# Performance work log

Hardware: AMD Instinct MI355X
Metric: run time of the kernel (lower is better)

## Reference

```python
import jax, jax.numpy as jnp
import numpy as np
import math

B, N, DIM = 4, 2048, 768
HEADS, DIM_HEAD = 12, 64
SCALE = math.sqrt(DIM_HEAD)


def setup_inputs() -> dict:
    key = jax.random.key(0)
    ks = jax.random.split(key, 5)
    inner = HEADS * DIM_HEAD
    x = jax.random.normal(ks[0], (B, N, DIM), dtype=jnp.float32)
    # Linear weights stored as [in, out] so y = x @ W (equivalent to torch Linear with W.T)
    w_q = jax.random.normal(ks[1], (DIM, inner), dtype=jnp.float32) * 0.02
    w_k = jax.random.normal(ks[2], (DIM, inner), dtype=jnp.float32) * 0.02
    w_v = jax.random.normal(ks[3], (DIM, inner), dtype=jnp.float32) * 0.02
    w_o = jax.random.normal(ks[4], (inner, DIM), dtype=jnp.float32) * 0.02
    b_o = jnp.zeros((DIM,), dtype=jnp.float32)
    return {"x": x, "w_q": w_q, "w_k": w_k, "w_v": w_v, "w_o": w_o, "b_o": b_o}


def _split_heads(t):
    # [b, n, h*d] -> [b, h, n, d]
    b, n, _ = t.shape
    return t.reshape(b, n, HEADS, DIM_HEAD).transpose(0, 2, 1, 3)


def reference(x, w_q, w_k, w_v, w_o, b_o):
    # context = x (self-attention, kv_include_self=False)
    q = _split_heads(x @ w_q)  # [b,h,n,d]
    k = _split_heads(x @ w_k)
    v = _split_heads(x @ w_v)
    scores = jnp.einsum("bhnd,bhmd->bhnm", q, k) / SCALE  # [b,h,n,n]
    attn = jax.nn.softmax(scores, axis=-1)  # dropout p=0 -> identity
    h = jnp.einsum("bhnm,bhmd->bhnd", attn, v)  # [b,h,n,d]
    H = h.transpose(0, 2, 1, 3).reshape(x.shape[0], x.shape[1], HEADS * DIM_HEAD)
    out = H @ w_o + b_o
    return out
```

## Files before the change

### kernel.cpp

```cpp
#include <hip/hip_runtime.h>
#include <hip/hip_bf16.h>
#include <cstdint>
#include <cstddef>

#define HEADS 12
#define DHEAD 64
#define SEQ   2048
#define DIMM  768
#define BATCH 4
#define MROWS (BATCH*SEQ)
#define BH    (BATCH*HEADS)
#define SCL_Q 0.18033688011112042f

typedef __attribute__((ext_vector_type(8))) short short8;
typedef __attribute__((ext_vector_type(4))) short short4v;
typedef __attribute__((ext_vector_type(4))) float floatx4;

__device__ __forceinline__ unsigned short f2bf(float f) {
    union { float f; uint32_t u; } v; v.f = f;
    uint32_t u = v.u;
    u += 0x7fffu + ((u >> 16) & 1u);
    return (unsigned short)(u >> 16);
}
__device__ __forceinline__ float bf2f(unsigned short h) {
    union { uint32_t u; float f; } v; v.u = ((uint32_t)h) << 16;
    return v.f;
}
__device__ __forceinline__ uint32_t pkbf(float a, float b) {
    __hip_bfloat162 h = __float22bfloat162_rn(make_float2(a, b));
    uint32_t u; __builtin_memcpy(&u, &h, 4); return u;
}
__device__ __forceinline__ float fexp2(float x) {
#if __has_builtin(__builtin_amdgcn_exp2f)
    return __builtin_amdgcn_exp2f(x);
#else
    return exp2f(x);
#endif
}

#if __has_builtin(__builtin_amdgcn_global_load_lds)
#define HAVE_GLDS 1
__device__ __forceinline__ void glds16(const unsigned short* g, unsigned short* l) {
    __builtin_amdgcn_global_load_lds(
        (const __attribute__((address_space(1))) unsigned int*)g,
        (__attribute__((address_space(3))) unsigned int*)l, 16, 0, 0);
}
#else
#define HAVE_GLDS 0
#endif

__device__ __forceinline__ int detect_f32(const uint32_t* xw, int tid) {
    __shared__ int cnt_;
    if (tid == 0) cnt_ = 0;
    __syncthreads();
    uint32_t w = xw[(size_t)(tid & 255) * 4096];
    float av = fabsf(bf2f((unsigned short)(w & 0xFFFFu)));
    atomicAdd(&cnt_, (av >= 9.0949e-13f && av <= 256.0f) ? 1 : 0);
    __syncthreads();
    return (cnt_ < 192) ? 1 : 0;
}

__global__ __launch_bounds__(256) void prep(
    const void* __restrict__ x,
    const void* __restrict__ wq, const void* __restrict__ wk,
    const void* __restrict__ wv, const void* __restrict__ wo,
    unsigned short* __restrict__ xc,
    unsigned short* __restrict__ wtq, unsigned short* __restrict__ wtk,
    unsigned short* __restrict__ wtv, unsigned short* __restrict__ wto)
{
    const int tid = threadIdx.x;
    const int isf32 = detect_f32((const uint32_t*)x, tid);
    const int blk = blockIdx.x;

    if (blk < 2304) {
        __shared__ unsigned short tile[32][33];
        const int m = blk / 576, rr = blk % 576;
        const void* src; unsigned short* dst;
        switch (m) {
            case 0: src = wq; dst = wtq; break;
            case 1: src = wk; dst = wtk; break;
            case 2: src = wv; dst = wtv; break;
            default: src = wo; dst = wto; break;
        }
        const float* srcf = (const float*)src;
        const unsigned short* srcs = (const unsigned short*)src;
        const int tx = tid & 31, ty = tid >> 5;
        const int k0 = (rr % 24) * 32;
        const int n0 = (rr / 24) * 32;
        #pragma unroll
        for (int it = 0; it < 4; it++) {
            int r = ty + it * 8;
            size_t idx = (size_t)(k0 + r) * DIMM + n0 + tx;
            tile[r][tx] = isf32 ? f2bf(srcf[idx]) : srcs[idx];
        }
        __syncthreads();
        #pragma unroll
        for (int it = 0; it < 4; it++) {
            int r = ty + it * 8;
            dst[(size_t)(n0 + r) * DIMM + k0 + tx] = tile[tx][r];
        }
    } else {
        const size_t i0 = ((size_t)(blk - 2304) * 256 + tid) * 8;
        if (isf32) {
            const float* xf = (const float*)x;
            float4 a = *(const float4*)&xf[i0];
            float4 b = *(const float4*)&xf[i0 + 4];
            short8 s = { (short)f2bf(a.x), (short)f2bf(a.y), (short)f2bf(a.z), (short)f2bf(a.w),
                         (short)f2bf(b.x), (short)f2bf(b.y), (short)f2bf(b.z), (short)f2bf(b.w) };
            *(short8*)&xc[i0] = s;
        } else {
            *(short8*)&xc[i0] = *(const short8*)&((const unsigned short*)x)[i0];
        }
    }
}

__global__ __launch_bounds__(256) void gemm_bt(
    const unsigned short* __restrict__ A,
    const unsigned short* __restrict__ Wt0,
    const unsigned short* __restrict__ Wt1,
    const unsigned short* __restrict__ Wt2,
    void* __restrict__ O0, void* __restrict__ O1, void* __restrict__ O2,
    const void* __restrict__ bias,
    const uint32_t* __restrict__ xsample,
    int mode_base)
{
    const int blk   = blockIdx.x;
    const int bmix  = blk & 63;
    const int inner = blk >> 6;
    int bnix, mode;
    if (mode_base == 0) { bnix = inner % 6; mode = inner / 6; }
    else                { bnix = inner;     mode = 3;         }

    const unsigned short* Wt = (mode == 1) ? Wt1 : (mode == 2) ? Wt2 : Wt0;
    void* OutV               = (mode == 1) ? O1  : (mode == 2) ? O2  : O0;
    unsigned short* Out16 = (unsigned short*)OutV;
    float* Outf           = (float*)OutV;

    int isf32 = 0;
    if (mode == 3) isf32 = detect_f32(xsample, threadIdx.x);

    __shared__ unsigned short As[128 * 64];
    __shared__ unsigned short Bs[128 * 64];

    const int tid  = threadIdx.x;
    const int wid  = tid >> 6;
    const int lane = tid & 63;
    const int l16  = lane & 15;
    const int quad = lane >> 4;
    const int wm   = wid & 1;
    const int wn   = wid >> 1;
    const int bm   = bmix * 128;
    const int bn   = bnix * 128;
    const bool swap = (mode != 2);

    floatx4 acc[4][4];
    #pragma unroll
    for (int i = 0; i < 4; i++)
        #pragma unroll
        for (int j = 0; j < 4; j++)
            acc[i][j] = floatx4{0.f, 0.f, 0.f, 0.f};

    for (int kk = 0; kk < DIMM; kk += 64) {
        #pragma unroll
        for (int t = 0; t < 4; t++) {
            const int c  = t * 256 + tid;
            const int r  = c >> 3;
            const int lc = (((c & 7) ^ (r & 7))) * 8;
#if HAVE_GLDS
            glds16(&A [(size_t)(bm + r) * DIMM + kk + lc], &As[(t * 256 + wid * 64) * 8]);
            glds16(&Wt[(size_t)(bn + r) * DIMM + kk + lc], &Bs[(t * 256 + wid * 64) * 8]);
#else
            *(short8*)&As[c * 8] = *(const short8*)&A [(size_t)(bm + r) * DIMM + kk + lc];
            *(short8*)&Bs[c * 8] = *(const short8*)&Wt[(size_t)(bn + r) * DIMM + kk + lc];
#endif
        }
        __syncthreads();
        #pragma unroll
        for (int ks = 0; ks < 2; ks++) {
            const int ph = ((ks * 4 + quad) ^ (l16 & 7)) * 8;
            short8 xa[4], wb[4];
            #pragma unroll
            for (int t = 0; t < 4; t++)
                xa[t] = *(const short8*)&As[(wm * 64 + t * 16 + l16) * 64 + ph];
            #pragma unroll
            for (int t = 0; t < 4; t++)
                wb[t] = *(const short8*)&Bs[(wn * 64 + t * 16 + l16) * 64 + ph];
            if (swap) {
                #pragma unroll
                for (int mt = 0; mt < 4; mt++)
                    #pragma unroll
                    for (int nt = 0; nt < 4; nt++)
                        acc[mt][nt] = __builtin_amdgcn_mfma_f32_16x16x32_bf16(
                            wb[mt], xa[nt], acc[mt][nt], 0, 0, 0);
            } else {
                #pragma unroll
                for (int mt = 0; mt < 4; mt++)
                    #pragma unroll
                    for (int nt = 0; nt < 4; nt++)
                        acc[mt][nt] = __builtin_amdgcn_mfma_f32_16x16x32_bf16(
                            xa[mt], wb[nt], acc[mt][nt], 0, 0, 0);
            }
        }
        __syncthreads();
    }

    if (!swap) {
        #pragma unroll
        for (int nt = 0; nt < 4; nt++) {
            const int gcol = bn + wn * 64 + nt * 16 + l16;
            #pragma unroll
            for (int mt = 0; mt < 4; mt++) {
                const int grow0 = bm + wm * 64 + mt * 16 + quad * 4;
                const int b = grow0 >> 11, n0 = grow0 & 2047;
                const int h = gcol >> 6,  d  = gcol & 63;
                size_t addr = ((size_t)(b * HEADS + h) * DHEAD + d) * SEQ + n0;
                short4v pk = { (short)f2bf(acc[mt][nt][0]), (short)f2bf(acc[mt][nt][1]),
                               (short)f2bf(acc[mt][nt][2]), (short)f2bf(acc[mt][nt][3]) };
                *(short4v*)&Out16[addr] = pk;
            }
        }
    } else {
        #pragma unroll
        for (int nt = 0; nt < 4; nt++) {
            const int grow = bm + wm * 64 + nt * 16 + l16;
            #pragma unroll
            for (int mt = 0; mt < 4; mt++) {
                const int gcol0 = bn + wn * 64 + mt * 16 + quad * 4;
                float v0 = acc[mt][nt][0], v1 = acc[mt][nt][1];
                float v2 = acc[mt][nt][2], v3 = acc[mt][nt][3];
                if (mode == 0) { v0 *= SCL_Q; v1 *= SCL_Q; v2 *= SCL_Q; v3 *= SCL_Q; }
                if (mode == 3) {
                    if (isf32) {
                        float4 bv = *(const float4*)&((const float*)bias)[gcol0];
                        float4 o = { v0 + bv.x, v1 + bv.y, v2 + bv.z, v3 + bv.w };
                        *(float4*)&Outf[(size_t)grow * DIMM + gcol0] = o;
                    } else {
                        const unsigned short* bb = &((const unsigned short*)bias)[gcol0];
                        short4v pk = { (short)f2bf(v0 + bf2f(bb[0])),
                                       (short)f2bf(v1 + bf2f(bb[1])),
                                       (short)f2bf(v2 + bf2f(bb[2])),
                                       (short)f2bf(v3 + bf2f(bb[3])) };
                        *(short4v*)&Out16[(size_t)grow * DIMM + gcol0] = pk;
                    }
                } else {
                    const int b = grow >> 11, n = grow & 2047;
                    const int h = gcol0 >> 6, d = gcol0 & 63;
                    size_t addr = ((size_t)(b * HEADS + h) * SEQ + n) * DHEAD + d;
                    short4v pk = { (short)f2bf(v0), (short)f2bf(v1),
                                   (short)f2bf(v2), (short)f2bf(v3) };
                    *(short4v*)&Out16[addr] = pk;
                }
            }
        }
    }
}

__global__ __launch_bounds__(256, 3) void attn(
    const unsigned short* __restrict__ Q,
    const unsigned short* __restrict__ K,
    const unsigned short* __restrict__ Vt,
    unsigned short* __restrict__ Hout)
{
    __shared__ unsigned short Ks[64 * 72];
    __shared__ unsigned short Vs[64 * 72];
    __shared__ unsigned short Ps[8][16 * 72];

    const int tid  = threadIdx.x;
    const int wid  = tid >> 6;
    const int lane = tid & 63;
    const int l16  = lane & 15;
    const int quad = lane >> 4;

    const int bh = blockIdx.x % BH;
    const int qt = blockIdx.x / BH;

    short8 qf[2][2];
    #pragma unroll
    for (int t = 0; t < 2; t++) {
        const int qrow = qt * 128 + wid * 32 + t * 16 + l16;
        const size_t qbase = ((size_t)bh * SEQ + qrow) * DHEAD;
        qf[t][0] = *(const short8*)&Q[qbase + quad * 8];
        qf[t][1] = *(const short8*)&Q[qbase + 32 + quad * 8];
    }

    const short8 ones = { (short)0x3F80, (short)0x3F80, (short)0x3F80, (short)0x3F80,
                          (short)0x3F80, (short)0x3F80, (short)0x3F80, (short)0x3F80 };

    floatx4 ot[2][4];
    floatx4 acc_l[2];
    #pragma unroll
    for (int t = 0; t < 2; t++) {
        acc_l[t] = floatx4{0.f, 0.f, 0.f, 0.f};
        #pragma unroll
        for (int i = 0; i < 4; i++) ot[t][i] = floatx4{0.f, 0.f, 0.f, 0.f};
    }

    const size_t kbase = (size_t)bh * SEQ * DHEAD;
    const size_t vbase = (size_t)bh * DHEAD * SEQ;

    short8 rk[2], rv[2];
    #pragma unroll
    for (int j = 0; j < 2; j++) {
        const int c = tid + j * 256, r = c >> 3, c8 = (c & 7) * 8;
        rk[j] = *(const short8*)&K[kbase + (size_t)r * DHEAD + c8];
        rv[j] = *(const short8*)&Vt[vbase + (size_t)r * SEQ + c8];
    }

    short8 vfr[2][4];
    short8 pfr[2][2];

    for (int kt = 0; kt < SEQ / 64; kt++) {
        if (kt > 0) {
            #pragma unroll
            for (int ks = 0; ks < 2; ks++) {
                #pragma unroll
                for (int dt = 0; dt < 4; dt++)
                    vfr[ks][dt] = *(const short8*)&Vs[(dt * 16 + l16) * 72 + ks * 32 + quad * 8];
                #pragma unroll
                for (int t = 0; t < 2; t++)
                    pfr[ks][t] = *(const short8*)&Ps[wid * 2 + t][l16 * 72 + ks * 32 + quad * 8];
            }
        }
        __syncthreads();
        #pragma unroll
        for (int j = 0; j < 2; j++) {
            const int c = tid + j * 256, r = c >> 3, c8 = (c & 7) * 8;
            *(short8*)&Ks[r * 72 + c8] = rk[j];
            *(short8*)&Vs[r * 72 + c8] = rv[j];
        }
        __syncthreads();
        if (kt + 1 < SEQ / 64) {
            #pragma unroll
            for (int j = 0; j < 2; j++) {
                const int c = tid + j * 256, r = c >> 3, c8 = (c & 7) * 8;
                rk[j] = *(const short8*)&K[kbase + (size_t)((kt + 1) * 64 + r) * DHEAD + c8];
                rv[j] = *(const short8*)&Vt[vbase + (size_t)r * SEQ + (kt + 1) * 64 + c8];
            }
        }

        uint2 pk[2][4];
        #pragma unroll
        for (int mt = 0; mt < 4; mt++) {
            short8 kf0 = *(const short8*)&Ks[(mt * 16 + l16) * 72 + quad * 8];
            short8 kf1 = *(const short8*)&Ks[(mt * 16 + l16) * 72 + 32 + quad * 8];
            #pragma unroll
            for (int t = 0; t < 2; t++) {
                floatx4 a = floatx4{0.f, 0.f, 0.f, 0.f};
                a = __builtin_amdgcn_mfma_f32_16x16x32_bf16(kf0, qf[t][0], a, 0, 0, 0);
                a = __builtin_amdgcn_mfma_f32_16x16x32_bf16(kf1, qf[t][1], a, 0, 0, 0);
                pk[t][mt] = (uint2){ pkbf(fexp2(a[0]), fexp2(a[1])),
                                     pkbf(fexp2(a[2]), fexp2(a[3])) };
            }
        }

        if (kt > 0) {
            #pragma unroll
            for (int ks = 0; ks < 2; ks++) {
                #pragma unroll
                for (int t = 0; t < 2; t++) {
                    #pragma unroll
                    for (int dt = 0; dt < 4; dt++)
                        ot[t][dt] = __builtin_amdgcn_mfma_f32_16x16x32_bf16(
                            vfr[ks][dt], pfr[ks][t], ot[t][dt], 0, 0, 0);
                    acc_l[t] = __builtin_amdgcn_mfma_f32_16x16x32_bf16(
                        ones, pfr[ks][t], acc_l[t], 0, 0, 0);
                }
            }
        }

        #pragma unroll
        for (int t = 0; t < 2; t++)
            #pragma unroll
            for (int mt = 0; mt < 4; mt++)
                *(uint2*)&Ps[wid * 2 + t][l16 * 72 + mt * 16 + quad * 4] = pk[t][mt];
    }

    {
        #pragma unroll
        for (int ks = 0; ks < 2; ks++) {
            #pragma unroll
            for (int dt = 0; dt < 4; dt++)
                vfr[ks][dt] = *(const short8*)&Vs[(dt * 16 + l16) * 72 + ks * 32 + quad * 8];
            #pragma unroll
            for (int t = 0; t < 2; t++)
                pfr[ks][t] = *(const short8*)&Ps[wid * 2 + t][l16 * 72 + ks * 32 + quad * 8];
        }
        #pragma unroll
        for (int ks = 0; ks < 2; ks++)
            #pragma unroll
            for (int t = 0; t < 2; t++) {
                #pragma unroll
                for (int dt = 0; dt < 4; dt++)
                    ot[t][dt] = __builtin_amdgcn_mfma_f32_16x16x32_bf16(
                        vfr[ks][dt], pfr[ks][t], ot[t][dt], 0, 0, 0);
                acc_l[t] = __builtin_amdgcn_mfma_f32_16x16x32_bf16(
                    ones, pfr[ks][t], acc_l[t], 0, 0, 0);
            }
    }

    const int b = bh / HEADS, h = bh % HEADS;
    #pragma unroll
    for (int t = 0; t < 2; t++) {
        const float inv_l = 1.0f / acc_l[t][0];
        unsigned short* Pw = Ps[wid * 2 + t];
        #pragma unroll
        for (int dt = 0; dt < 4; dt++) {
            uint2 pk2 = { pkbf(ot[t][dt][0] * inv_l, ot[t][dt][1] * inv_l),
                          pkbf(ot[t][dt][2] * inv_l, ot[t][dt][3] * inv_l) };
            *(uint2*)&Pw[l16 * 72 + dt * 16 + quad * 4] = pk2;
        }
        const int q_r   = lane >> 2;
        const int dpart = (lane & 3) * 16;
        short8 h0 = *(const short8*)&Pw[q_r * 72 + dpart];
        short8 h1 = *(const short8*)&Pw[q_r * 72 + dpart + 8];
        const int growg = b * SEQ + qt * 128 + wid * 32 + t * 16 + q_r;
        const size_t oaddr = (size_t)growg * DIMM + h * DHEAD + dpart;
        *(short8*)&Hout[oaddr] = h0;
        *(short8*)&Hout[oaddr + 8] = h1;
    }
}

extern "C" void kernel_launch(void* const* d_in, const int* in_sizes, int n_in,
                              void* d_out, int out_size, void* d_ws, size_t ws_size,
                              hipStream_t stream)
{
    (void)in_sizes; (void)n_in; (void)out_size;
    const void* x  = d_in[0];
    const void* wq = d_in[1];
    const void* wk = d_in[2];
    const void* wv = d_in[3];
    const void* wo = d_in[4];
    const void* bo = d_in[5];

    char* ws = (char*)d_ws;
    const size_t SZ_QKV = (size_t)MROWS * DIMM * sizeof(unsigned short);
    const size_t SZ_W   = (size_t)DIMM * DIMM * sizeof(unsigned short);
    const size_t need = 5 * SZ_QKV + 4 * SZ_W;
    if (ws_size < need) return;

    unsigned short* xc   = (unsigned short*)(ws);
    unsigned short* Qws  = (unsigned short*)(ws + 1 * SZ_QKV);
    unsigned short* Kws  = (unsigned short*)(ws + 2 * SZ_QKV);
    unsigned short* Vtws = (unsigned short*)(ws + 3 * SZ_QKV);
    unsigned short* Hws  = (unsigned short*)(ws + 4 * SZ_QKV);
    unsigned short* Wtq  = (unsigned short*)(ws + 5 * SZ_QKV);
    unsigned short* Wtk  = (unsigned short*)(ws + 5 * SZ_QKV + SZ_W);
    unsigned short* Wtv  = (unsigned short*)(ws + 5 * SZ_QKV + 2 * SZ_W);
    unsigned short* Wto  = (unsigned short*)(ws + 5 * SZ_QKV + 3 * SZ_W);

    hipLaunchKernelGGL(prep, dim3(2304 + MROWS * DIMM / 2048), dim3(256), 0, stream,
                       x, wq, wk, wv, wo, xc, Wtq, Wtk, Wtv, Wto);
    hipLaunchKernelGGL(gemm_bt, dim3(64 * 18), dim3(256), 0, stream,
                       xc, Wtq, Wtk, Wtv, (void*)Qws, (void*)Kws, (void*)Vtws,
                       bo, (const uint32_t*)x, 0);
    hipLaunchKernelGGL(attn, dim3(BH * (SEQ / 128)), dim3(256), 0, stream,
                       Qws, Kws, Vtws, Hws);
    hipLaunchKernelGGL(gemm_bt, dim3(64 * 6), dim3(256), 0, stream,
                       Hws, Wto, Wto, Wto, d_out, d_out, d_out,
                       bo, (const uint32_t*)x, 3);
}
```

Measured before the change: 244.9 us.

## Split GEMM into QKV and output kernels; use 256-row tiles for QKV

```diff
diff --git a/kernel.cpp b/kernel.cpp
--- a/kernel.cpp
+++ b/kernel.cpp
@@ -114,30 +114,158 @@
     }
 }
 
-__global__ __launch_bounds__(256) void gemm_bt(
+__global__ __launch_bounds__(256) void gemm_qkv(
     const unsigned short* __restrict__ A,
     const unsigned short* __restrict__ Wt0,
     const unsigned short* __restrict__ Wt1,
     const unsigned short* __restrict__ Wt2,
-    void* __restrict__ O0, void* __restrict__ O1, void* __restrict__ O2,
+    unsigned short* __restrict__ O0,
+    unsigned short* __restrict__ O1,
+    unsigned short* __restrict__ O2)
+{
+    const int blk   = blockIdx.x;
+    const int bmix  = blk & 31;
+    const int inner = blk >> 5;
+    const int bnix  = inner % 6;
+    const int mode  = inner / 6;
+
+    const unsigned short* Wt = (mode == 1) ? Wt1 : (mode == 2) ? Wt2 : Wt0;
+    unsigned short* Out      = (mode == 1) ? O1  : (mode == 2) ? O2  : O0;
+
+    __shared__ unsigned short As[256 * 64];
+    __shared__ unsigned short Bs[128 * 64];
+
+    const int tid  = threadIdx.x;
+    const int wid  = tid >> 6;
+    const int lane = tid & 63;
+    const int l16  = lane & 15;
+    const int quad = lane >> 4;
+    const int wm   = wid & 1;
+    const int wn   = wid >> 1;
+    const int bm   = bmix * 256;
+    const int bn   = bnix * 128;
+    const bool swap = (mode != 2);
+
+    floatx4 acc[2][4][4];
+    #pragma unroll
+    for (int s = 0; s < 2; s++)
+        #pragma unroll
+        for (int i = 0; i < 4; i++)
+            #pragma unroll
+            for (int j = 0; j < 4; j++)
+                acc[s][i][j] = floatx4{0.f, 0.f, 0.f, 0.f};
+
+    for (int kk = 0; kk < DIMM; kk += 64) {
+        #pragma unroll
+        for (int t = 0; t < 8; t++) {
+            const int c  = t * 256 + tid;
+            const int r  = c >> 3;
+            const int lc = (((c & 7) ^ (r & 7))) * 8;
+#if HAVE_GLDS
+            glds16(&A[(size_t)(bm + r) * DIMM + kk + lc], &As[(t * 256 + wid * 64) * 8]);
+#else
+            *(short8*)&As[c * 8] = *(const short8*)&A[(size_t)(bm + r) * DIMM + kk + lc];
+#endif
+        }
+        #pragma unroll
+        for (int t = 0; t < 4; t++) {
+            const int c  = t * 256 + tid;
+            const int r  = c >> 3;
+            const int lc = (((c & 7) ^ (r & 7))) * 8;
+#if HAVE_GLDS
+            glds16(&Wt[(size_t)(bn + r) * DIMM + kk + lc], &Bs[(t * 256 + wid * 64) * 8]);
+#else
+            *(short8*)&Bs[c * 8] = *(const short8*)&Wt[(size_t)(bn + r) * DIMM + kk + lc];
+#endif
+        }
+        __syncthreads();
+        #pragma unroll
+        for (int ks = 0; ks < 2; ks++) {
+            const int ph = ((ks * 4 + quad) ^ (l16 & 7)) * 8;
+            short8 wb[4];
+            #pragma unroll
+            for (int t = 0; t < 4; t++)
+                wb[t] = *(const short8*)&Bs[(wn * 64 + t * 16 + l16) * 64 + ph];
+            #pragma unroll
+            for (int s = 0; s < 2; s++) {
+                short8 xa[4];
+                #pragma unroll
+                for (int t = 0; t < 4; t++)
+                    xa[t] = *(const short8*)&As[(s * 128 + wm * 64 + t * 16 + l16) * 64 + ph];
+                if (swap) {
+                    #pragma unroll
+                    for (int mt = 0; mt < 4; mt++)
+                        #pragma unroll
+                        for (int nt = 0; nt < 4; nt++)
+                            acc[s][mt][nt] = __builtin_amdgcn_mfma_f32_16x16x32_bf16(
+                                wb[mt], xa[nt], acc[s][mt][nt], 0, 0, 0);
+                } else {
+                    #pragma unroll
+                    for (int mt = 0; mt < 4; mt++)
+                        #pragma unroll
+                        for (int nt = 0; nt < 4; nt++)
+                            acc[s][mt][nt] = __builtin_amdgcn_mfma_f32_16x16x32_bf16(
+                                xa[mt], wb[nt], acc[s][mt][nt], 0, 0, 0);
+                }
+            }
+        }
+        __syncthreads();
+    }
+
+    #pragma unroll
+    for (int s = 0; s < 2; s++) {
+        const int bms = bm + s * 128;
+        if (!swap) {
+            #pragma unroll
+            for (int nt = 0; nt < 4; nt++) {
+                const int gcol = bn + wn * 64 + nt * 16 + l16;
+                #pragma unroll
+                for (int mt = 0; mt < 4; mt++) {
+                    const int grow0 = bms + wm * 64 + mt * 16 + quad * 4;
+                    const int b = grow0 >> 11, n0 = grow0 & 2047;
+                    const int h = gcol >> 6,  d  = gcol & 63;
+                    size_t addr = ((size_t)(b * HEADS + h) * DHEAD + d) * SEQ + n0;
+                    short4v pk = { (short)f2bf(acc[s][mt][nt][0]), (short)f2bf(acc[s][mt][nt][1]),
+                                   (short)f2bf(acc[s][mt][nt][2]), (short)f2bf(acc[s][mt][nt][3]) };
+                    *(short4v*)&Out[addr] = pk;
+                }
+            }
+        } else {
+            #pragma unroll
+            for (int nt = 0; nt < 4; nt++) {
+                const int grow = bms + wm * 64 + nt * 16 + l16;
+                #pragma unroll
+                for (int mt = 0; mt < 4; mt++) {
+                    const int gcol0 = bn + wn * 64 + mt * 16 + quad * 4;
+                    float v0 = acc[s][mt][nt][0], v1 = acc[s][mt][nt][1];
+                    float v2 = acc[s][mt][nt][2], v3 = acc[s][mt][nt][3];
+                    if (mode == 0) { v0 *= SCL_Q; v1 *= SCL_Q; v2 *= SCL_Q; v3 *= SCL_Q; }
+                    const int b = grow >> 11, n = grow & 2047;
+                    const int h = gcol0 >> 6, d = gcol0 & 63;
+                    size_t addr = ((size_t)(b * HEADS + h) * SEQ + n) * DHEAD + d;
+                    short4v pk = { (short)f2bf(v0), (short)f2bf(v1),
+                                   (short)f2bf(v2), (short)f2bf(v3) };
+                    *(short4v*)&Out[addr] = pk;
+                }
+            }
+        }
+    }
+}
+
+__global__ __launch_bounds__(256) void gemm_out(
+    const unsigned short* __restrict__ A,
+    const unsigned short* __restrict__ Wt,
+    void* __restrict__ OutV,
     const void* __restrict__ bias,
-    const uint32_t* __restrict__ xsample,
-    int mode_base)
+    const uint32_t* __restrict__ xsample)
 {
     const int blk   = blockIdx.x;
     const int bmix  = blk & 63;
-    const int inner = blk >> 6;
-    int bnix, mode;
-    if (mode_base == 0) { bnix = inner % 6; mode = inner / 6; }
-    else                { bnix = inner;     mode = 3;         }
-
-    const unsigned short* Wt = (mode == 1) ? Wt1 : (mode == 2) ? Wt2 : Wt0;
-    void* OutV               = (mode == 1) ? O1  : (mode == 2) ? O2  : O0;
+    const int bnix  = blk >> 6;
+
     unsigned short* Out16 = (unsigned short*)OutV;
     float* Outf           = (float*)OutV;
-
-    int isf32 = 0;
-    if (mode == 3) isf32 = detect_f32(xsample, threadIdx.x);
+    const int isf32 = detect_f32(xsample, threadIdx.x);
 
     __shared__ unsigned short As[128 * 64];
     __shared__ unsigned short Bs[128 * 64];
@@ -151,7 +279,6 @@
     const int wn   = wid >> 1;
     const int bm   = bmix * 128;
     const int bn   = bnix * 128;
-    const bool swap = (mode != 2);
 
     floatx4 acc[4][4];
     #pragma unroll
@@ -185,71 +312,35 @@
             #pragma unroll
             for (int t = 0; t < 4; t++)
                 wb[t] = *(const short8*)&Bs[(wn * 64 + t * 16 + l16) * 64 + ph];
-            if (swap) {
-                #pragma unroll
-                for (int mt = 0; mt < 4; mt++)
-                    #pragma unroll
-                    for (int nt = 0; nt < 4; nt++)
-                        acc[mt][nt] = __builtin_amdgcn_mfma_f32_16x16x32_bf16(
-                            wb[mt], xa[nt], acc[mt][nt], 0, 0, 0);
+            #pragma unroll
+            for (int mt = 0; mt < 4; mt++)
+                #pragma unroll
+                for (int nt = 0; nt < 4; nt++)
+                    acc[mt][nt] = __builtin_amdgcn_mfma_f32_16x16x32_bf16(
+                        wb[mt], xa[nt], acc[mt][nt], 0, 0, 0);
+        }
+        __syncthreads();
+    }
+
+    #pragma unroll
+    for (int nt = 0; nt < 4; nt++) {
+        const int grow = bm + wn * 0 + wm * 64 + nt * 16 + l16;
+        #pragma unroll
+        for (int mt = 0; mt < 4; mt++) {
+            const int gcol0 = bn + wn * 64 + mt * 16 + quad * 4;
+            float v0 = acc[mt][nt][0], v1 = acc[mt][nt][1];
+            float v2 = acc[mt][nt][2], v3 = acc[mt][nt][3];
+            if (isf32) {
+                float4 bv = *(const float4*)&((const float*)bias)[gcol0];
+                float4 o = { v0 + bv.x, v1 + bv.y, v2 + bv.z, v3 + bv.w };
+                *(float4*)&Outf[(size_t)grow * DIMM + gcol0] = o;
             } else {
-                #pragma unroll
-                for (int mt = 0; mt < 4; mt++)
-                    #pragma unroll
-                    for (int nt = 0; nt < 4; nt++)
-                        acc[mt][nt] = __builtin_amdgcn_mfma_f32_16x16x32_bf16(
-                            xa[mt], wb[nt], acc[mt][nt], 0, 0, 0);
-            }
-        }
-        __syncthreads();
-    }
-
-    if (!swap) {
-        #pragma unroll
-        for (int nt = 0; nt < 4; nt++) {
-            const int gcol = bn + wn * 64 + nt * 16 + l16;
-            #pragma unroll
-            for (int mt = 0; mt < 4; mt++) {
-                const int grow0 = bm + wm * 64 + mt * 16 + quad * 4;
-                const int b = grow0 >> 11, n0 = grow0 & 2047;
-                const int h = gcol >> 6,  d  = gcol & 63;
-                size_t addr = ((size_t)(b * HEADS + h) * DHEAD + d) * SEQ + n0;
-                short4v pk = { (short)f2bf(acc[mt][nt][0]), (short)f2bf(acc[mt][nt][1]),
-                               (short)f2bf(acc[mt][nt][2]), (short)f2bf(acc[mt][nt][3]) };
-                *(short4v*)&Out16[addr] = pk;
-            }
-        }
-    } else {
-        #pragma unroll
-        for (int nt = 0; nt < 4; nt++) {
-            const int grow = bm + wm * 64 + nt * 16 + l16;
-            #pragma unroll
-            for (int mt = 0; mt < 4; mt++) {
-                const int gcol0 = bn + wn * 64 + mt * 16 + quad * 4;
-                float v0 = acc[mt][nt][0], v1 = acc[mt][nt][1];
-                float v2 = acc[mt][nt][2], v3 = acc[mt][nt][3];
-                if (mode == 0) { v0 *= SCL_Q; v1 *= SCL_Q; v2 *= SCL_Q; v3 *= SCL_Q; }
-                if (mode == 3) {
-                    if (isf32) {
-                        float4 bv = *(const float4*)&((const float*)bias)[gcol0];
-                        float4 o = { v0 + bv.x, v1 + bv.y, v2 + bv.z, v3 + bv.w };
-                        *(float4*)&Outf[(size_t)grow * DIMM + gcol0] = o;
-                    } else {
-                        const unsigned short* bb = &((const unsigned short*)bias)[gcol0];
-                        short4v pk = { (short)f2bf(v0 + bf2f(bb[0])),
-                                       (short)f2bf(v1 + bf2f(bb[1])),
-                                       (short)f2bf(v2 + bf2f(bb[2])),
-                                       (short)f2bf(v3 + bf2f(bb[3])) };
-                        *(short4v*)&Out16[(size_t)grow * DIMM + gcol0] = pk;
-                    }
-                } else {
-                    const int b = grow >> 11, n = grow & 2047;
-                    const int h = gcol0 >> 6, d = gcol0 & 63;
-                    size_t addr = ((size_t)(b * HEADS + h) * SEQ + n) * DHEAD + d;
-                    short4v pk = { (short)f2bf(v0), (short)f2bf(v1),
-                                   (short)f2bf(v2), (short)f2bf(v3) };
-                    *(short4v*)&Out16[addr] = pk;
-                }
+                const unsigned short* bb = &((const unsigned short*)bias)[gcol0];
+                short4v pk = { (short)f2bf(v0 + bf2f(bb[0])),
+                               (short)f2bf(v1 + bf2f(bb[1])),
+                               (short)f2bf(v2 + bf2f(bb[2])),
+                               (short)f2bf(v3 + bf2f(bb[3])) };
+                *(short4v*)&Out16[(size_t)grow * DIMM + gcol0] = pk;
             }
         }
     }
@@ -450,12 +541,10 @@
 
     hipLaunchKernelGGL(prep, dim3(2304 + MROWS * DIMM / 2048), dim3(256), 0, stream,
                        x, wq, wk, wv, wo, xc, Wtq, Wtk, Wtv, Wto);
-    hipLaunchKernelGGL(gemm_bt, dim3(64 * 18), dim3(256), 0, stream,
-                       xc, Wtq, Wtk, Wtv, (void*)Qws, (void*)Kws, (void*)Vtws,
-                       bo, (const uint32_t*)x, 0);
+    hipLaunchKernelGGL(gemm_qkv, dim3(32 * 18), dim3(256), 0, stream,
+                       xc, Wtq, Wtk, Wtv, Qws, Kws, Vtws);
     hipLaunchKernelGGL(attn, dim3(BH * (SEQ / 128)), dim3(256), 0, stream,
                        Qws, Kws, Vtws, Hws);
-    hipLaunchKernelGGL(gemm_bt, dim3(64 * 6), dim3(256), 0, stream,
-                       Hws, Wto, Wto, Wto, d_out, d_out, d_out,
-                       bo, (const uint32_t*)x, 3);
-}
+    hipLaunchKernelGGL(gemm_out, dim3(64 * 6), dim3(256), 0, stream,
+                       Hws, Wto, d_out, bo, (const uint32_t*)x);
+}
```

Result: slower. 261.0 us (+6.6%).
